# Kernel tuning notes

Hardware: AMD Instinct MI355X
Metric: run time of the kernel (lower is better)

## Reference

```python
import jax, jax.numpy as jnp
import numpy as np

D_MODEL = 1024
NUM_HEAD = 16
D_HEAD = D_MODEL // NUM_HEAD
NEG_INF = -1e9


def setup_inputs() -> dict:
    key = jax.random.key(0)
    ks = jax.random.split(key, 10)
    B, S = 16, 512
    v = jax.random.normal(ks[0], (B, S, D_MODEL), dtype=jnp.float32)
    lengths = jax.random.randint(ks[1], (B,), 1, S + 1, dtype=jnp.int32)
    scale = 0.02
    Wq = jax.random.normal(ks[2], (D_MODEL, D_MODEL), dtype=jnp.float32) * scale
    bq = jnp.zeros((D_MODEL,), dtype=jnp.float32)
    Wk = jax.random.normal(ks[3], (D_MODEL, D_MODEL), dtype=jnp.float32) * scale
    bk = jnp.zeros((D_MODEL,), dtype=jnp.float32)
    Wv = jax.random.normal(ks[4], (D_MODEL, D_MODEL), dtype=jnp.float32) * scale
    bv = jnp.zeros((D_MODEL,), dtype=jnp.float32)
    Wo = jax.random.normal(ks[5], (D_MODEL, D_MODEL), dtype=jnp.float32) * scale
    bo = jnp.zeros((D_MODEL,), dtype=jnp.float32)
    return {"v": v, "lengths": lengths, "Wq": Wq, "bq": bq, "Wk": Wk,
            "bk": bk, "Wv": Wv, "bv": bv, "Wo": Wo, "bo": bo}


def reference(v, lengths, Wq, bq, Wk, bk, Wv, bv, Wo, bo):
    B, S, D = v.shape
    H, Dh = NUM_HEAD, D_HEAD
    # key-padding mask: True where key position j is valid (j < lengths[b])
    valid = jnp.arange(S)[None, :] < lengths[:, None]          # [B, S]
    # project q, k, v and split heads -> [B, H, S, Dh]
    def split_heads(x):
        return x.reshape(B, S, H, Dh).transpose(0, 2, 1, 3)
    q = split_heads(v @ Wq + bq)
    k = split_heads(v @ Wk + bk)
    val = split_heads(v @ Wv + bv)
    scores = jnp.einsum('bhqd,bhkd->bhqk', q, k) / jnp.sqrt(jnp.float32(Dh))
    scores = jnp.where(valid[:, None, None, :], scores, NEG_INF)  # mask padded keys
    attn = jax.nn.softmax(scores, axis=-1)
    out = jnp.einsum('bhqk,bhkd->bhqd', attn, val)              # [B, H, S, Dh]
    out = out.transpose(0, 2, 1, 3).reshape(B, S, D)
    return out @ Wo + bo
```

## Files before the change

kernel.cpp:

```cpp
#include <hip/hip_runtime.h>
#include <hip/hip_bf16.h>

typedef unsigned short u16;
typedef __attribute__((ext_vector_type(8))) short short8;
typedef __attribute__((ext_vector_type(4))) float f32x4;

#define B_SZ 16
#define S_SZ 512
#define D_SZ 1024
#define H_SZ 16
#define DH_SZ 64
#define M_SZ (B_SZ * S_SZ)
#define EXPSCALE 0.18033688f

__device__ __forceinline__ void gload_lds16(const void* g, void* l) {
  __builtin_amdgcn_global_load_lds(
      (const __attribute__((address_space(1))) unsigned int*)g,
      (__attribute__((address_space(3))) unsigned int*)l,
      16, 0, 0);
}

__global__ __launch_bounds__(256) void prep(
    const float* __restrict__ v, u16* __restrict__ vB,
    const float* __restrict__ W0, const float* __restrict__ W1,
    const float* __restrict__ W2, const float* __restrict__ W3,
    u16* __restrict__ T0, u16* __restrict__ T1,
    u16* __restrict__ T2, u16* __restrict__ T3) {
  __shared__ float tile[32][33];
  const int bid = blockIdx.x;
  if (bid < 8192) {
    int i = bid * 256 + threadIdx.x;
    const float4 f = *(const float4*)&v[(size_t)i * 4];
    ushort4 o; __hip_bfloat16 h;
    h = __float2bfloat16(f.x); o.x = *(u16*)&h;
    h = __float2bfloat16(f.y); o.y = *(u16*)&h;
    h = __float2bfloat16(f.z); o.z = *(u16*)&h;
    h = __float2bfloat16(f.w); o.w = *(u16*)&h;
    *(ushort4*)&vB[(size_t)i * 4] = o;
    return;
  }
  const int tb = bid - 8192;
  const int z = tb >> 10, rem = tb & 1023;
  const int by = rem >> 5, bx = rem & 31;
  const float* W; u16* T;
  switch (z) {
    case 0: W = W0; T = T0; break;
    case 1: W = W1; T = T1; break;
    case 2: W = W2; T = T2; break;
    default: W = W3; T = T3; break;
  }
  int tx = threadIdx.x & 31, ty = threadIdx.x >> 5;
  int x = bx * 32 + tx;
#pragma unroll
  for (int i = 0; i < 32; i += 8)
    tile[ty + i][tx] = W[(size_t)(by * 32 + ty + i) * 1024 + x];
  __syncthreads();
  int x2 = by * 32 + tx;
#pragma unroll
  for (int i = 0; i < 32; i += 8) {
    __hip_bfloat16 h = __float2bfloat16(tile[tx][ty + i]);
    T[(size_t)(bx * 32 + ty + i) * 1024 + x2] = *(u16*)&h;
  }
}

struct G8 {
  const u16* A; const u16* Bt;
  u16* As; u16* Bs;
  int m0, n0;
  int wave, c, quad, r7, wm, wn;
  int srow, slc8;
};

#define AS_T (128 * 64)
#define BS_T (256 * 64)

__device__ __forceinline__ void stage_a(const G8& g, int buf, int kt, int i) {
  const int grp = g.wave * 2 + i;
  gload_lds16(&g.A[(size_t)(g.m0 + grp * 8 + g.srow) * 1024 + kt * 64 + g.slc8],
              g.As + buf * AS_T + grp * 512);
}
__device__ __forceinline__ void stage_b(const G8& g, int buf, int kt, int i) {
  const int grp = g.wave * 4 + i;
  gload_lds16(&g.Bt[(size_t)(g.n0 + grp * 8 + g.srow) * 1024 + kt * 64 + g.slc8],
              g.Bs + buf * BS_T + grp * 512);
}

template<bool ST, int VM>
__device__ __forceinline__ void tile_step(const G8& g, int cur, int stg, int kt2,
                                          f32x4 acc[4][4]) {
  const u16* ab = g.As + cur * AS_T;
  const u16* bb = g.Bs + cur * BS_T;
  short8 af[4], bf[4];

  {
    const int pc = (g.quad ^ g.r7) * 8;
#pragma unroll
    for (int i = 0; i < 4; ++i) {
      af[i] = *(const short8*)&ab[(g.wm + i * 16 + g.c) * 64 + pc];
      bf[i] = *(const short8*)&bb[(g.wn + i * 16 + g.c) * 64 + pc];
    }
    if constexpr (ST) {
      stage_a(g, stg, kt2, 0);
      stage_a(g, stg, kt2, 1);
      stage_b(g, stg, kt2, 0);
    }
    __builtin_amdgcn_s_barrier();
    __builtin_amdgcn_s_setprio(1);
#pragma unroll
    for (int mi = 0; mi < 4; ++mi)
#pragma unroll
      for (int ni = 0; ni < 4; ++ni)
        acc[mi][ni] = __builtin_amdgcn_mfma_f32_16x16x32_bf16(
            af[mi], bf[ni], acc[mi][ni], 0, 0, 0);
    __builtin_amdgcn_s_setprio(0);
    __builtin_amdgcn_s_barrier();
  }

  {
    const int pc = ((4 + g.quad) ^ g.r7) * 8;
#pragma unroll
    for (int i = 0; i < 4; ++i) {
      af[i] = *(const short8*)&ab[(g.wm + i * 16 + g.c) * 64 + pc];
      bf[i] = *(const short8*)&bb[(g.wn + i * 16 + g.c) * 64 + pc];
    }
    if constexpr (ST) {
      stage_b(g, stg, kt2, 1);
      stage_b(g, stg, kt2, 2);
      stage_b(g, stg, kt2, 3);
    }
    __builtin_amdgcn_s_barrier();
    __builtin_amdgcn_s_setprio(1);
#pragma unroll
    for (int mi = 0; mi < 4; ++mi)
#pragma unroll
      for (int ni = 0; ni < 4; ++ni)
        acc[mi][ni] = __builtin_amdgcn_mfma_f32_16x16x32_bf16(
            af[mi], bf[ni], acc[mi][ni], 0, 0, 0);
    __builtin_amdgcn_s_setprio(0);
    if constexpr (VM == 6) {
      asm volatile("s_waitcnt vmcnt(6)" ::: "memory");
      __builtin_amdgcn_s_barrier();
    } else if constexpr (VM == 0) {
      asm volatile("s_waitcnt vmcnt(0)" ::: "memory");
      __builtin_amdgcn_s_barrier();
    }
  }
}

__device__ __forceinline__ void gemm_core8(
    const u16* __restrict__ A, const u16* __restrict__ Bt,
    u16* AsB, u16* BsB, int m0, int n0, f32x4 acc[4][4]) {
  const int tid = threadIdx.x;
  const int lane = tid & 63;
  G8 g;
  g.A = A; g.Bt = Bt; g.As = AsB; g.Bs = BsB;
  g.m0 = m0; g.n0 = n0;
  g.wave = tid >> 6;
  g.c = lane & 15; g.quad = lane >> 4; g.r7 = g.c & 7;
  g.wm = (g.wave >> 2) * 64;
  g.wn = (g.wave & 3) * 64;
  g.srow = lane >> 3;
  g.slc8 = ((lane & 7) ^ g.srow) * 8;

  stage_a(g, 0, 0, 0); stage_a(g, 0, 0, 1);
  stage_b(g, 0, 0, 0); stage_b(g, 0, 0, 1); stage_b(g, 0, 0, 2); stage_b(g, 0, 0, 3);
  stage_a(g, 1, 1, 0); stage_a(g, 1, 1, 1);
  stage_b(g, 1, 1, 0); stage_b(g, 1, 1, 1); stage_b(g, 1, 1, 2); stage_b(g, 1, 1, 3);
  asm volatile("s_waitcnt vmcnt(6)" ::: "memory");
  __builtin_amdgcn_s_barrier();

  int cur = 0, stg = 2;
#pragma unroll 1
  for (int t = 0; t < 14; ++t) {
    tile_step<true, 6>(g, cur, stg, t + 2, acc);
    cur = (cur == 2) ? 0 : cur + 1;
    stg = (stg == 2) ? 0 : stg + 1;
  }
  tile_step<false, 0>(g, cur, 0, 0, acc);
  tile_step<false, -1>(g, 0, 0, 0, acc);
}

template<int Z>
__global__ __launch_bounds__(512, 2) void gemm_split(
    const u16* __restrict__ A, const u16* __restrict__ Bt,
    const float* __restrict__ bias, u16* __restrict__ Out) {
  __shared__ u16 As[3][AS_T];
  __shared__ u16 Bs[3][BS_T];
  const int m0 = blockIdx.x * 128, n0 = blockIdx.y * 256;

  f32x4 acc[4][4];
#pragma unroll
  for (int i = 0; i < 4; ++i)
#pragma unroll
    for (int j = 0; j < 4; ++j) acc[i][j] = f32x4{0.f, 0.f, 0.f, 0.f};

  gemm_core8(A, Bt, &As[0][0], &Bs[0][0], m0, n0, acc);

  const int lane = threadIdx.x & 63, wave = threadIdx.x >> 6;
  const int wm = (wave >> 2) * 64, wn = (wave & 3) * 64;
  const int c = lane & 15, quad = lane >> 4;
#pragma unroll
  for (int ni = 0; ni < 4; ++ni) {
    int n = n0 + wn + ni * 16 + c;
    float bval = bias[n];
#pragma unroll
    for (int mi = 0; mi < 4; ++mi) {
      int mb = m0 + wm + mi * 16 + quad * 4;
      if constexpr (Z == 2) {
        int bb = mb >> 9, s = mb & 511, hh = n >> 6, d = n & 63;
        ushort4 st;
        __hip_bfloat16 h0 = __float2bfloat16(acc[mi][ni][0] + bval); st.x = *(u16*)&h0;
        __hip_bfloat16 h1 = __float2bfloat16(acc[mi][ni][1] + bval); st.y = *(u16*)&h1;
        __hip_bfloat16 h2 = __float2bfloat16(acc[mi][ni][2] + bval); st.z = *(u16*)&h2;
        __hip_bfloat16 h3 = __float2bfloat16(acc[mi][ni][3] + bval); st.w = *(u16*)&h3;
        *(ushort4*)&Out[(((size_t)(bb * 16 + hh) * 64 + d) << 9) + s] = st;
      } else {
#pragma unroll
        for (int r = 0; r < 4; ++r) {
          int m = mb + r;
          float val = acc[mi][ni][r] + bval;
          if constexpr (Z == 0) val *= EXPSCALE;
          __hip_bfloat16 hb = __float2bfloat16(val);
          if constexpr (Z == 0) {
            Out[(size_t)m * 1024 + n] = *(u16*)&hb;
          } else {
            int bb = m >> 9, s = m & 511, hh = n >> 6, d = n & 63;
            Out[(((size_t)(bb * 16 + hh) * 512 + s) << 6) + d] = *(u16*)&hb;
          }
        }
      }
    }
  }
}

__global__ __launch_bounds__(512, 2) void gemm_out(
    const u16* __restrict__ A, const u16* __restrict__ Bt,
    const float* __restrict__ bias, float* __restrict__ Cf) {
  __shared__ u16 As[3][AS_T];
  __shared__ u16 Bs[3][BS_T];
  const int m0 = blockIdx.x * 128, n0 = blockIdx.y * 256;

  f32x4 acc[4][4];
#pragma unroll
  for (int i = 0; i < 4; ++i)
#pragma unroll
    for (int j = 0; j < 4; ++j) acc[i][j] = f32x4{0.f, 0.f, 0.f, 0.f};

  gemm_core8(A, Bt, &As[0][0], &Bs[0][0], m0, n0, acc);

  const int lane = threadIdx.x & 63, wave = threadIdx.x >> 6;
  const int wm = (wave >> 2) * 64, wn = (wave & 3) * 64;
  const int c = lane & 15, quad = lane >> 4;
#pragma unroll
  for (int ni = 0; ni < 4; ++ni) {
    int n = n0 + wn + ni * 16 + c;
    float bval = bias[n];
#pragma unroll
    for (int mi = 0; mi < 4; ++mi) {
#pragma unroll
      for (int r = 0; r < 4; ++r) {
        int m = m0 + wm + mi * 16 + quad * 4 + r;
        Cf[(size_t)m * 1024 + n] = acc[mi][ni][r] + bval;
      }
    }
  }
}

__global__ __launch_bounds__(256) void attn_v8(
    const u16* __restrict__ Q, const u16* __restrict__ Kt,
    const u16* __restrict__ Vt, const int* __restrict__ lengths,
    u16* __restrict__ O) {
  const int qc = blockIdx.x, h = blockIdx.y, b = blockIdx.z;
  const int t = threadIdx.x;
  const int lane = t & 63, wave = t >> 6;
  const int c = lane & 15, quad = lane >> 4;
  const int kb = quad * 8;
  const int len = lengths[b];
  const int q0 = qc * 128 + wave * 32;

  __shared__ __align__(16) u16 Ks[64 * 64];
  __shared__ __align__(16) u16 Vs[64 * 64];
  __shared__ __align__(16) u16 Pt[4][32 * 72];

  const size_t bBase = (size_t)b * (S_SZ * D_SZ);
  const size_t hBase = ((size_t)(b * H_SZ + h)) * (S_SZ * DH_SZ);

  short8 aq[2][2];
#pragma unroll
  for (int qt = 0; qt < 2; ++qt) {
    aq[qt][0] = *(const short8*)&Q[bBase + (size_t)(q0 + qt * 16 + c) * 1024 + h * 64 + kb];
    aq[qt][1] = *(const short8*)&Q[bBase + (size_t)(q0 + qt * 16 + c) * 1024 + h * 64 + 32 + kb];
  }

  const short ONE = (short)0x3F80;
  const short8 ones = {ONE, ONE, ONE, ONE, ONE, ONE, ONE, ONE};

  const int srow = lane >> 3;
  const int slc = (lane & 7) ^ srow;

  f32x4 o[2][4];
  f32x4 osum[2];
#pragma unroll
  for (int qt = 0; qt < 2; ++qt) {
    osum[qt] = f32x4{0.f, 0.f, 0.f, 0.f};
#pragma unroll
    for (int i = 0; i < 4; ++i) o[qt][i] = f32x4{0.f, 0.f, 0.f, 0.f};
  }

  const int kmax = (len + 63) & ~63;
  for (int k0 = 0; k0 < kmax; k0 += 64) {
    __syncthreads();
#pragma unroll
    for (int g = 0; g < 2; ++g) {
      const int rb = (wave * 2 + g) * 8;
      gload_lds16(&Kt[hBase + (size_t)(k0 + rb + srow) * 64 + slc * 8],
                  &Ks[(wave * 2 + g) * 512]);
      gload_lds16(&Vt[hBase + (size_t)(rb + srow) * 512 + k0 + slc * 8],
                  &Vs[(wave * 2 + g) * 512]);
    }
    __syncthreads();

    const bool full = (k0 + 64 <= len);

#pragma unroll
    for (int sub = 0; sub < 4; ++sub) {
      const int row = sub * 16 + c;
      short8 bk0 = *(const short8*)&Ks[row * 64 + ((quad ^ (c & 7))) * 8];
      short8 bk1 = *(const short8*)&Ks[row * 64 + (((4 + quad) ^ (c & 7))) * 8];
      const int keyb = k0 + sub * 16 + quad * 4;
#pragma unroll
      for (int qt = 0; qt < 2; ++qt) {
        f32x4 s = {0.f, 0.f, 0.f, 0.f};
        s = __builtin_amdgcn_mfma_f32_16x16x32_bf16(bk0, aq[qt][0], s, 0, 0, 0);
        s = __builtin_amdgcn_mfma_f32_16x16x32_bf16(bk1, aq[qt][1], s, 0, 0, 0);
        float p0, p1, p2, p3;
        if (full) {
          p0 = exp2f(s[0]); p1 = exp2f(s[1]);
          p2 = exp2f(s[2]); p3 = exp2f(s[3]);
        } else {
          p0 = (keyb + 0) < len ? exp2f(s[0]) : 0.f;
          p1 = (keyb + 1) < len ? exp2f(s[1]) : 0.f;
          p2 = (keyb + 2) < len ? exp2f(s[2]) : 0.f;
          p3 = (keyb + 3) < len ? exp2f(s[3]) : 0.f;
        }
        ushort4 st;
        __hip_bfloat16 h0 = __float2bfloat16(p0); st.x = *(u16*)&h0;
        __hip_bfloat16 h1 = __float2bfloat16(p1); st.y = *(u16*)&h1;
        __hip_bfloat16 h2 = __float2bfloat16(p2); st.z = *(u16*)&h2;
        __hip_bfloat16 h3 = __float2bfloat16(p3); st.w = *(u16*)&h3;
        *(ushort4*)&Pt[wave][(qt * 16 + c) * 72 + sub * 16 + quad * 4] = st;
      }
    }
#pragma unroll
    for (int ksub = 0; ksub < 2; ++ksub) {
      const short8 pa0 = *(const short8*)&Pt[wave][(c) * 72 + ksub * 32 + kb];
      const short8 pa1 = *(const short8*)&Pt[wave][(16 + c) * 72 + ksub * 32 + kb];
      osum[0] = __builtin_amdgcn_mfma_f32_16x16x32_bf16(pa0, ones, osum[0], 0, 0, 0);
      osum[1] = __builtin_amdgcn_mfma_f32_16x16x32_bf16(pa1, ones, osum[1], 0, 0, 0);
#pragma unroll
      for (int dt = 0; dt < 4; ++dt) {
        const int vrow = dt * 16 + c;
        short8 vb = *(const short8*)&Vs[vrow * 64 + (((ksub * 4 + quad) ^ (c & 7))) * 8];
        o[0][dt] = __builtin_amdgcn_mfma_f32_16x16x32_bf16(pa0, vb, o[0][dt], 0, 0, 0);
        o[1][dt] = __builtin_amdgcn_mfma_f32_16x16x32_bf16(pa1, vb, o[1][dt], 0, 0, 0);
      }
    }
  }

#pragma unroll
  for (int qt = 0; qt < 2; ++qt) {
    float inv[4];
#pragma unroll
    for (int r = 0; r < 4; ++r) inv[r] = 1.0f / osum[qt][r];
#pragma unroll
    for (int dt = 0; dt < 4; ++dt) {
#pragma unroll
      for (int r = 0; r < 4; ++r) {
        int s = q0 + qt * 16 + quad * 4 + r;
        float val = o[qt][dt][r] * inv[r];
        __hip_bfloat16 ob = __float2bfloat16(val);
        O[bBase + (size_t)s * 1024 + h * 64 + dt * 16 + c] = *(u16*)&ob;
      }
    }
  }
}

extern "C" void kernel_launch(void* const* d_in, const int* in_sizes, int n_in,
                              void* d_out, int out_size, void* d_ws, size_t ws_size,
                              hipStream_t stream) {
  const float* v  = (const float*)d_in[0];
  const int* lengths = (const int*)d_in[1];
  const float* Wq = (const float*)d_in[2];
  const float* bq = (const float*)d_in[3];
  const float* Wk = (const float*)d_in[4];
  const float* bk = (const float*)d_in[5];
  const float* Wv = (const float*)d_in[6];
  const float* bv = (const float*)d_in[7];
  const float* Wo = (const float*)d_in[8];
  const float* bo = (const float*)d_in[9];

  char* ws = (char*)d_ws;
  const size_t TSZ = (size_t)M_SZ * D_SZ * 2;
  const size_t WSZ = (size_t)1 << 21;
  u16* vB  = (u16*)(ws);
  u16* AO  = vB;
  u16* WqT = (u16*)(ws + TSZ + 0 * WSZ);
  u16* WkT = (u16*)(ws + TSZ + 1 * WSZ);
  u16* WvT = (u16*)(ws + TSZ + 2 * WSZ);
  u16* WoT = (u16*)(ws + TSZ + 3 * WSZ);
  u16* Qb  = (u16*)(ws + TSZ + 4 * WSZ + 0 * TSZ);
  u16* Kt  = (u16*)(ws + TSZ + 4 * WSZ + 1 * TSZ);
  u16* Vt  = (u16*)(ws + TSZ + 4 * WSZ + 2 * TSZ);

  prep<<<dim3(8192 + 4096), 256, 0, stream>>>(v, vB, Wq, Wk, Wv, Wo, WqT, WkT, WvT, WoT);

  gemm_split<0><<<dim3(64, 4), 512, 0, stream>>>(vB, WqT, bq, Qb);
  gemm_split<1><<<dim3(64, 4), 512, 0, stream>>>(vB, WkT, bk, Kt);
  gemm_split<2><<<dim3(64, 4), 512, 0, stream>>>(vB, WvT, bv, Vt);

  attn_v8<<<dim3(4, 16, 16), 256, 0, stream>>>(Qb, Kt, Vt, lengths, AO);

  gemm_out<<<dim3(64, 4), 512, 0, stream>>>(AO, WoT, bo, (float*)d_out);
}
```

Baseline: 219.7 us.

## Permute K rows so softmax probabilities feed PV MFMA directly from registers

K tiles are now loaded into shared memory with a permuted row order. With that order, the score MFMA output lanes hold exactly the probability elements each lane needs as the A operand of the P·V MFMA. The probabilities are packed into registers instead of going through a per-wave shared-memory Pt buffer, which removes the LDS store and reload and frees LDS. The mask key indices are remapped to match. The remaining changes factor the bf16 conversion into a helper.

```diff
diff --git a/kernel.cpp b/kernel.cpp
--- a/kernel.cpp
+++ b/kernel.cpp
@@ -2,8 +2,10 @@
 #include <hip/hip_bf16.h>
 
 typedef unsigned short u16;
+typedef unsigned int u32;
 typedef __attribute__((ext_vector_type(8))) short short8;
 typedef __attribute__((ext_vector_type(4))) float f32x4;
+typedef __attribute__((ext_vector_type(4))) unsigned int u32x4;
 
 #define B_SZ 16
 #define S_SZ 512
@@ -18,6 +20,11 @@
       (const __attribute__((address_space(1))) unsigned int*)g,
       (__attribute__((address_space(3))) unsigned int*)l,
       16, 0, 0);
+}
+
+__device__ __forceinline__ u16 bf16b(float x) {
+  __hip_bfloat16 h = __float2bfloat16(x);
+  return *(u16*)&h;
 }
 
 __global__ __launch_bounds__(256) void prep(
@@ -31,11 +38,8 @@
   if (bid < 8192) {
     int i = bid * 256 + threadIdx.x;
     const float4 f = *(const float4*)&v[(size_t)i * 4];
-    ushort4 o; __hip_bfloat16 h;
-    h = __float2bfloat16(f.x); o.x = *(u16*)&h;
-    h = __float2bfloat16(f.y); o.y = *(u16*)&h;
-    h = __float2bfloat16(f.z); o.z = *(u16*)&h;
-    h = __float2bfloat16(f.w); o.w = *(u16*)&h;
+    ushort4 o;
+    o.x = bf16b(f.x); o.y = bf16b(f.y); o.z = bf16b(f.z); o.w = bf16b(f.w);
     *(ushort4*)&vB[(size_t)i * 4] = o;
     return;
   }
@@ -57,10 +61,8 @@
   __syncthreads();
   int x2 = by * 32 + tx;
 #pragma unroll
-  for (int i = 0; i < 32; i += 8) {
-    __hip_bfloat16 h = __float2bfloat16(tile[tx][ty + i]);
-    T[(size_t)(bx * 32 + ty + i) * 1024 + x2] = *(u16*)&h;
-  }
+  for (int i = 0; i < 32; i += 8)
+    T[(size_t)(bx * 32 + ty + i) * 1024 + x2] = bf16b(tile[tx][ty + i]);
 }
 
 struct G8 {
@@ -209,10 +211,10 @@
       if constexpr (Z == 2) {
         int bb = mb >> 9, s = mb & 511, hh = n >> 6, d = n & 63;
         ushort4 st;
-        __hip_bfloat16 h0 = __float2bfloat16(acc[mi][ni][0] + bval); st.x = *(u16*)&h0;
-        __hip_bfloat16 h1 = __float2bfloat16(acc[mi][ni][1] + bval); st.y = *(u16*)&h1;
-        __hip_bfloat16 h2 = __float2bfloat16(acc[mi][ni][2] + bval); st.z = *(u16*)&h2;
-        __hip_bfloat16 h3 = __float2bfloat16(acc[mi][ni][3] + bval); st.w = *(u16*)&h3;
+        st.x = bf16b(acc[mi][ni][0] + bval);
+        st.y = bf16b(acc[mi][ni][1] + bval);
+        st.z = bf16b(acc[mi][ni][2] + bval);
+        st.w = bf16b(acc[mi][ni][3] + bval);
         *(ushort4*)&Out[(((size_t)(bb * 16 + hh) * 64 + d) << 9) + s] = st;
       } else {
 #pragma unroll
@@ -220,12 +222,11 @@
           int m = mb + r;
           float val = acc[mi][ni][r] + bval;
           if constexpr (Z == 0) val *= EXPSCALE;
-          __hip_bfloat16 hb = __float2bfloat16(val);
           if constexpr (Z == 0) {
-            Out[(size_t)m * 1024 + n] = *(u16*)&hb;
+            Out[(size_t)m * 1024 + n] = bf16b(val);
           } else {
             int bb = m >> 9, s = m & 511, hh = n >> 6, d = n & 63;
-            Out[(((size_t)(bb * 16 + hh) * 512 + s) << 6) + d] = *(u16*)&hb;
+            Out[(((size_t)(bb * 16 + hh) * 512 + s) << 6) + d] = bf16b(val);
           }
         }
       }
@@ -266,7 +267,7 @@
   }
 }
 
-__global__ __launch_bounds__(256) void attn_v8(
+__global__ __launch_bounds__(256) void attn_v9(
     const u16* __restrict__ Q, const u16* __restrict__ Kt,
     const u16* __restrict__ Vt, const int* __restrict__ lengths,
     u16* __restrict__ O) {
@@ -274,13 +275,11 @@
   const int t = threadIdx.x;
   const int lane = t & 63, wave = t >> 6;
   const int c = lane & 15, quad = lane >> 4;
-  const int kb = quad * 8;
   const int len = lengths[b];
   const int q0 = qc * 128 + wave * 32;
 
   __shared__ __align__(16) u16 Ks[64 * 64];
   __shared__ __align__(16) u16 Vs[64 * 64];
-  __shared__ __align__(16) u16 Pt[4][32 * 72];
 
   const size_t bBase = (size_t)b * (S_SZ * D_SZ);
   const size_t hBase = ((size_t)(b * H_SZ + h)) * (S_SZ * DH_SZ);
@@ -288,8 +287,8 @@
   short8 aq[2][2];
 #pragma unroll
   for (int qt = 0; qt < 2; ++qt) {
-    aq[qt][0] = *(const short8*)&Q[bBase + (size_t)(q0 + qt * 16 + c) * 1024 + h * 64 + kb];
-    aq[qt][1] = *(const short8*)&Q[bBase + (size_t)(q0 + qt * 16 + c) * 1024 + h * 64 + 32 + kb];
+    aq[qt][0] = *(const short8*)&Q[bBase + (size_t)(q0 + qt * 16 + c) * 1024 + h * 64 + quad * 8];
+    aq[qt][1] = *(const short8*)&Q[bBase + (size_t)(q0 + qt * 16 + c) * 1024 + h * 64 + 32 + quad * 8];
   }
 
   const short ONE = (short)0x3F80;
@@ -312,55 +311,59 @@
     __syncthreads();
 #pragma unroll
     for (int g = 0; g < 2; ++g) {
-      const int rb = (wave * 2 + g) * 8;
-      gload_lds16(&Kt[hBase + (size_t)(k0 + rb + srow) * 64 + slc * 8],
-                  &Ks[(wave * 2 + g) * 512]);
-      gload_lds16(&Vt[hBase + (size_t)(rb + srow) * 512 + k0 + slc * 8],
-                  &Vs[(wave * 2 + g) * 512]);
+      const int grp = wave * 2 + g;
+      const int rho = grp * 8 + srow;
+      const int grow = ((rho >> 4) & 1) * 32 + ((rho >> 2) & 3) * 8 +
+                       ((rho >> 5) & 1) * 4 + (rho & 3);
+      gload_lds16(&Kt[hBase + (size_t)(k0 + grow) * 64 + slc * 8],
+                  &Ks[grp * 512]);
+      gload_lds16(&Vt[hBase + (size_t)(grp * 8 + srow) * 512 + k0 + slc * 8],
+                  &Vs[grp * 512]);
     }
     __syncthreads();
 
     const bool full = (k0 + 64 <= len);
 
 #pragma unroll
-    for (int sub = 0; sub < 4; ++sub) {
-      const int row = sub * 16 + c;
-      short8 bk0 = *(const short8*)&Ks[row * 64 + ((quad ^ (c & 7))) * 8];
-      short8 bk1 = *(const short8*)&Ks[row * 64 + (((4 + quad) ^ (c & 7))) * 8];
-      const int keyb = k0 + sub * 16 + quad * 4;
-#pragma unroll
-      for (int qt = 0; qt < 2; ++qt) {
-        f32x4 s = {0.f, 0.f, 0.f, 0.f};
-        s = __builtin_amdgcn_mfma_f32_16x16x32_bf16(bk0, aq[qt][0], s, 0, 0, 0);
-        s = __builtin_amdgcn_mfma_f32_16x16x32_bf16(bk1, aq[qt][1], s, 0, 0, 0);
-        float p0, p1, p2, p3;
-        if (full) {
-          p0 = exp2f(s[0]); p1 = exp2f(s[1]);
-          p2 = exp2f(s[2]); p3 = exp2f(s[3]);
-        } else {
-          p0 = (keyb + 0) < len ? exp2f(s[0]) : 0.f;
-          p1 = (keyb + 1) < len ? exp2f(s[1]) : 0.f;
-          p2 = (keyb + 2) < len ? exp2f(s[2]) : 0.f;
-          p3 = (keyb + 3) < len ? exp2f(s[3]) : 0.f;
+    for (int half = 0; half < 2; ++half) {
+      u32 pk[2][4];
+#pragma unroll
+      for (int ss = 0; ss < 2; ++ss) {
+        const int sub = half + ss * 2;
+        const int row = sub * 16 + c;
+        short8 bk0 = *(const short8*)&Ks[row * 64 + ((quad ^ (c & 7))) * 8];
+        short8 bk1 = *(const short8*)&Ks[row * 64 + (((4 + quad) ^ (c & 7))) * 8];
+        const int keyb = k0 + (sub & 1) * 32 + quad * 8 + (sub >> 1) * 4;
+#pragma unroll
+        for (int qt = 0; qt < 2; ++qt) {
+          f32x4 s = {0.f, 0.f, 0.f, 0.f};
+          s = __builtin_amdgcn_mfma_f32_16x16x32_bf16(bk0, aq[qt][0], s, 0, 0, 0);
+          s = __builtin_amdgcn_mfma_f32_16x16x32_bf16(bk1, aq[qt][1], s, 0, 0, 0);
+          float p0, p1, p2, p3;
+          if (full) {
+            p0 = exp2f(s[0]); p1 = exp2f(s[1]);
+            p2 = exp2f(s[2]); p3 = exp2f(s[3]);
+          } else {
+            p0 = (keyb + 0) < len ? exp2f(s[0]) : 0.f;
+            p1 = (keyb + 1) < len ? exp2f(s[1]) : 0.f;
+            p2 = (keyb + 2) < len ? exp2f(s[2]) : 0.f;
+            p3 = (keyb + 3) < len ? exp2f(s[3]) : 0.f;
+          }
+          pk[qt][ss * 2 + 0] = (u32)bf16b(p0) | ((u32)bf16b(p1) << 16);
+          pk[qt][ss * 2 + 1] = (u32)bf16b(p2) | ((u32)bf16b(p3) << 16);
         }
-        ushort4 st;
-        __hip_bfloat16 h0 = __float2bfloat16(p0); st.x = *(u16*)&h0;
-        __hip_bfloat16 h1 = __float2bfloat16(p1); st.y = *(u16*)&h1;
-        __hip_bfloat16 h2 = __float2bfloat16(p2); st.z = *(u16*)&h2;
-        __hip_bfloat16 h3 = __float2bfloat16(p3); st.w = *(u16*)&h3;
-        *(ushort4*)&Pt[wave][(qt * 16 + c) * 72 + sub * 16 + quad * 4] = st;
       }
-    }
-#pragma unroll
-    for (int ksub = 0; ksub < 2; ++ksub) {
-      const short8 pa0 = *(const short8*)&Pt[wave][(c) * 72 + ksub * 32 + kb];
-      const short8 pa1 = *(const short8*)&Pt[wave][(16 + c) * 72 + ksub * 32 + kb];
+      u32x4 w0 = {pk[0][0], pk[0][1], pk[0][2], pk[0][3]};
+      u32x4 w1 = {pk[1][0], pk[1][1], pk[1][2], pk[1][3]};
+      short8 pa0, pa1;
+      __builtin_memcpy(&pa0, &w0, 16);
+      __builtin_memcpy(&pa1, &w1, 16);
       osum[0] = __builtin_amdgcn_mfma_f32_16x16x32_bf16(pa0, ones, osum[0], 0, 0, 0);
       osum[1] = __builtin_amdgcn_mfma_f32_16x16x32_bf16(pa1, ones, osum[1], 0, 0, 0);
 #pragma unroll
       for (int dt = 0; dt < 4; ++dt) {
         const int vrow = dt * 16 + c;
-        short8 vb = *(const short8*)&Vs[vrow * 64 + (((ksub * 4 + quad) ^ (c & 7))) * 8];
+        short8 vb = *(const short8*)&Vs[vrow * 64 + (((half * 4 + quad) ^ (c & 7))) * 8];
         o[0][dt] = __builtin_amdgcn_mfma_f32_16x16x32_bf16(pa0, vb, o[0][dt], 0, 0, 0);
         o[1][dt] = __builtin_amdgcn_mfma_f32_16x16x32_bf16(pa1, vb, o[1][dt], 0, 0, 0);
       }
@@ -378,8 +381,7 @@
       for (int r = 0; r < 4; ++r) {
         int s = q0 + qt * 16 + quad * 4 + r;
         float val = o[qt][dt][r] * inv[r];
-        __hip_bfloat16 ob = __float2bfloat16(val);
-        O[bBase + (size_t)s * 1024 + h * 64 + dt * 16 + c] = *(u16*)&ob;
+        O[bBase + (size_t)s * 1024 + h * 64 + dt * 16 + c] = bf16b(val);
       }
     }
   }
@@ -418,7 +420,7 @@
   gemm_split<1><<<dim3(64, 4), 512, 0, stream>>>(vB, WkT, bk, Kt);
   gemm_split<2><<<dim3(64, 4), 512, 0, stream>>>(vB, WvT, bv, Vt);
 
-  attn_v8<<<dim3(4, 16, 16), 256, 0, stream>>>(Qb, Kt, Vt, lengths, AO);
+  attn_v9<<<dim3(4, 16, 16), 256, 0, stream>>>(Qb, Kt, Vt, lengths, AO);
 
   gemm_out<<<dim3(64, 4), 512, 0, stream>>>(AO, WoT, bo, (float*)d_out);
 }
```

Measured after the change: 225.9 us. 1.03x slower.
